# Performance work log

Measured on AMD Instinct MI355X. Metric: run time of the kernel, lower is better.

The kernel has to match this reference:

```python
import jax, jax.numpy as jnp
import numpy as np

N, B, T, D, H = 200, 100, 256, 5, 20  # count_lstms, batch, seq_len, io units, lstm units


def setup_inputs() -> dict:
    key = jax.random.key(0)
    ks = jax.random.split(key, 4)
    inputs = jax.random.normal(ks[0], (B, T, D), dtype=jnp.float32)
    # Stacked per-LSTM parameters (Keras gate order: i, f, c, o)
    W = jax.random.normal(ks[1], (N, D, 4 * H), dtype=jnp.float32) * (1.0 / np.sqrt(D))
    U = jax.random.normal(ks[2], (N, H, 4 * H), dtype=jnp.float32) * (1.0 / np.sqrt(H))
    b = jnp.zeros((N, 4 * H), dtype=jnp.float32)
    dense_W = jax.random.normal(ks[3], (N * H, D), dtype=jnp.float32) * (1.0 / np.sqrt(N * H))
    dense_b = jnp.zeros((D,), dtype=jnp.float32)
    return {"inputs": inputs, "W": W, "U": U, "b": b, "dense_W": dense_W, "dense_b": dense_b}


def reference(inputs, W, U, b, dense_W, dense_b):
    # inputs: [B, T, D]; W: [N, D, 4H]; U: [N, H, 4H]; b: [N, 4H]
    n, h = W.shape[0], U.shape[1]
    batch = inputs.shape[0]
    x_t = jnp.transpose(inputs, (1, 0, 2))  # [T, B, D]
    h0 = jnp.zeros((n, batch, h), dtype=inputs.dtype)
    c0 = jnp.zeros((n, batch, h), dtype=inputs.dtype)

    def step(carry, xt):
        hprev, cprev = carry
        # gates for all N lstms at once: [N, B, 4H]
        z = (jnp.einsum('bd,ndk->nbk', xt, W)
             + jnp.einsum('nbh,nhk->nbk', hprev, U)
             + b[:, None, :])
        zi, zf, zg, zo = jnp.split(z, 4, axis=-1)
        i = jax.nn.sigmoid(zi)
        f = jax.nn.sigmoid(zf)
        g = jnp.tanh(zg)
        o = jax.nn.sigmoid(zo)
        cnew = f * cprev + i * g
        hnew = o * jnp.tanh(cnew)
        return (hnew, cnew), hnew

    (_, _), hs = jax.lax.scan(step, (h0, c0), x_t)  # hs: [T, N, B, H]
    # concat along feature axis -> [B, T, N*H]
    concat = jnp.transpose(hs, (2, 0, 1, 3)).reshape(batch, x_t.shape[0], n * h)
    out = concat @ dense_W + dense_b  # [B, T, D]
    return out
```

## Files before the change

### kernel.cpp

```cpp
#include <hip/hip_runtime.h>
#include <math.h>

constexpr int NL = 200;
constexpr int B  = 100;
constexpr int T  = 256;
constexpr int D  = 5;
constexpr int H  = 20;
constexpr int NW = 7;
constexpr int KP = 40;
constexpr int NWAVE = 5;
constexpr int BLKT  = 64 * NWAVE;

constexpr int KX = 24;

typedef float  f32x4  __attribute__((ext_vector_type(4)));
typedef short  bf16x8 __attribute__((ext_vector_type(8)));

__device__ __forceinline__ float rcpf(float x) { return __builtin_amdgcn_rcpf(x); }

#if __has_builtin(__builtin_amdgcn_exp2f)
__device__ __forceinline__ float exp2fast(float x) { return __builtin_amdgcn_exp2f(x); }
#else
__device__ __forceinline__ float exp2fast(float x) { return __expf(x * 0.6931471805599453f); }
#endif

__device__ __forceinline__ unsigned short f2bf(float f) {
    union { float f; unsigned u; } v; v.f = f;
    unsigned r = v.u + 0x7fffu + ((v.u >> 16) & 1u);
    return (unsigned short)(r >> 16);
}

__device__ __forceinline__ void block_sync_lds() {
    asm volatile("s_waitcnt lgkmcnt(0)" ::: "memory");
    __builtin_amdgcn_s_barrier();
}

constexpr float NLOG2E = -1.4426950408889634f;
constexpr float TLOG2E = 2.8853900817779268f;

__global__ __launch_bounds__(256) void init_out_kernel(const float* __restrict__ dense_b,
                                                       float* __restrict__ out, int n) {
    int i = blockIdx.x * 256 + threadIdx.x;
    if (i < n) out[i] = dense_b[i % D];
}

template<bool USE_WS>
__global__ __attribute__((amdgpu_flat_work_group_size(BLKT, BLKT)))
void lstm_mfma5_kernel(
    const float* __restrict__ x,
    const float* __restrict__ Wg,
    const float* __restrict__ Ug,
    const float* __restrict__ bg,
    const float* __restrict__ dWg,
    float* __restrict__ pw,
    float* __restrict__ out)
{
    const int blk = blockIdx.x;
    const int n   = blk / NW;
    const int w   = blk % NW;
    const int tid = threadIdx.x;
    const int wid = tid >> 6;
    const int l   = tid & 63;
    const int c16 = l & 15;
    const int g4  = l >> 4;

    __shared__ __align__(16) short bcol[2][16][KP];

    for (int i = tid; i < 2 * 16 * KP / 2; i += BLKT)
        ((int*)&bcol[0][0][0])[i] = 0;

    const float* Un = Ug  + (size_t)n * H * 4 * H;
    const float* Wn = Wg  + (size_t)n * D * 4 * H;
    const float* bn = bg  + (size_t)n * 4 * H;
    const float* dn = dWg + (size_t)n * H * D;

    const int gateA = c16 & 3;
    const int hA4   = c16 >> 2;
    const float sA  = (gateA == 2) ? TLOG2E : NLOG2E;
    const int colA  = gateA * H + (wid * 4 + hA4);
    bf16x8 afrag;
    #pragma unroll
    for (int j = 0; j < 8; ++j) {
        const int k = 8 * g4 + j;
        float v = 0.0f;
        if (k < KX) {
            const int mt = k % 6, gg = k / 6;
            if (mt < 5) v = Un[(mt * 4 + gg) * 4 * H + colA];
        } else if (k < KX + D) {
            v = Wn[(k - KX) * 4 * H + colA];
        } else if (k == 30) {
            v = bn[colA];
        }
        afrag[j] = (short)f2bf(sA * v);
    }
    bf16x8 afrag_d = {};
    if (wid == 1) {
        #pragma unroll
        for (int j = 0; j < 8; ++j) {
            const int k = 8 * g4 + j;
            float v = 0.0f;
            if (c16 < D && k < KX) {
                const int mt = k % 6, gg = k / 6;
                if (mt < 5) v = dn[(mt * 4 + gg) * D + c16];
            }
            afrag_d[j] = (short)f2bf(v);
        }
    }

    const int  bgl    = w * 16 + c16;
    const bool bvalid = bgl < B;
    const float* xp   = x + (size_t)(bvalid ? bgl : 0) * T * D;
    float* pwn = USE_WS ? (pw + (size_t)n * T * (D * B))
                        : (out + ((size_t)bgl * T) * D);

    __syncthreads();

    float xn[D];
    if (wid == 0 && l < 16) {
        bf16x8 xb;
        #pragma unroll
        for (int d = 0; d < D; ++d) xb[d] = (short)f2bf(xp[d]);
        xb[5] = 0; xb[6] = (short)0x3F80; xb[7] = 0;
        *(bf16x8*)&bcol[0][c16][KX] = xb;
        const float* x1 = xp + (size_t)((T > 1) ? 1 : 0) * D;
        #pragma unroll
        for (int d = 0; d < D; ++d) xn[d] = x1[d];
    }
    __syncthreads();

    float cst = 0.0f;
    const f32x4 zero4 = {0.0f, 0.0f, 0.0f, 0.0f};
    int p = 0;

    for (int t = 0; t < T; ++t) {
        const bf16x8 bfrag = *(const bf16x8*)&bcol[p][c16][8 * g4];

        if (wid == 1) {
            const f32x4 accd = __builtin_amdgcn_mfma_f32_16x16x32_bf16(
                afrag_d, bfrag, zero4, 0, 0, 0);
            if (t > 0 && bvalid) {
                #pragma unroll
                for (int reg = 0; reg < 4; ++reg) {
                    const int d = g4 * 4 + reg;
                    if (d < D) {
                        if (USE_WS)
                            pwn[(size_t)(t - 1) * (D * B) + d * B + bgl] = accd[reg];
                        else
                            atomicAdd(&pwn[(size_t)(t - 1) * D + d], accd[reg]);
                    }
                }
            }
        }

        const f32x4 acc = __builtin_amdgcn_mfma_f32_16x16x32_bf16(
            afrag, bfrag, zero4, 0, 0, 0);
        const float iv = rcpf(1.0f + exp2fast(acc[0]));
        const float fv = rcpf(1.0f + exp2fast(acc[1]));
        const float gv = fmaf(-2.0f, rcpf(exp2fast(acc[2]) + 1.0f), 1.0f);
        const float ov = rcpf(1.0f + exp2fast(acc[3]));
        cst = fmaf(fv, cst, iv * gv);
        const float th = fmaf(-2.0f, rcpf(exp2fast(TLOG2E * cst) + 1.0f), 1.0f);
        const float hv = ov * th;

        bcol[p ^ 1][c16][g4 * 6 + wid] = (short)f2bf(hv);

        if (wid == 0 && l < 16) {
            bf16x8 xb;
            #pragma unroll
            for (int d = 0; d < D; ++d) xb[d] = (short)f2bf(xn[d]);
            xb[5] = 0; xb[6] = (short)0x3F80; xb[7] = 0;
            *(bf16x8*)&bcol[p ^ 1][c16][KX] = xb;
            const float* x2 = xp + (size_t)((t + 2 < T) ? t + 2 : T - 1) * D;
            #pragma unroll
            for (int d = 0; d < D; ++d) xn[d] = x2[d];
        }

        block_sync_lds();
        p ^= 1;
    }

    if (wid == 1) {
        const bf16x8 bfrag = *(const bf16x8*)&bcol[p][c16][8 * g4];
        const f32x4 accd = __builtin_amdgcn_mfma_f32_16x16x32_bf16(
            afrag_d, bfrag, zero4, 0, 0, 0);
        if (bvalid) {
            #pragma unroll
            for (int reg = 0; reg < 4; ++reg) {
                const int d = g4 * 4 + reg;
                if (d < D) {
                    if (USE_WS)
                        pwn[(size_t)(T - 1) * (D * B) + d * B + bgl] = accd[reg];
                    else
                        atomicAdd(&pwn[(size_t)(T - 1) * D + d], accd[reg]);
                }
            }
        }
    }
}

__global__ __launch_bounds__(512) void reduce_kernel(
    const float* __restrict__ pw, const float* __restrict__ dense_b,
    float* __restrict__ out)
{
    const int t    = blockIdx.x;
    const int flat = threadIdx.x;
    if (flat >= B * D) return;
    const int d = flat / B;
    const int b = flat % B;
    const float* p = pw + (size_t)t * (D * B) + flat;
    constexpr size_t stride = (size_t)T * D * B;
    float a0 = 0.0f, a1 = 0.0f;
    #pragma unroll 10
    for (int n = 0; n < NL; n += 2) {
        a0 += p[(size_t)n * stride];
        a1 += p[(size_t)(n + 1) * stride];
    }
    out[((size_t)b * T + t) * D + d] = a0 + a1 + dense_b[d];
}

extern "C" void kernel_launch(void* const* d_in, const int* in_sizes, int n_in,
                              void* d_out, int out_size, void* d_ws, size_t ws_size,
                              hipStream_t stream) {
    const float* x   = (const float*)d_in[0];
    const float* Wg  = (const float*)d_in[1];
    const float* Ug  = (const float*)d_in[2];
    const float* bg  = (const float*)d_in[3];
    const float* dWg = (const float*)d_in[4];
    const float* dbv = (const float*)d_in[5];
    float* out = (float*)d_out;

    const size_t need = (size_t)NL * T * D * B * sizeof(float);
    if (ws_size >= need) {
        float* pw = (float*)d_ws;
        lstm_mfma5_kernel<true><<<NL * NW, BLKT, 0, stream>>>(x, Wg, Ug, bg, dWg, pw, out);
        reduce_kernel<<<T, 512, 0, stream>>>(pw, dbv, out);
    } else {
        init_out_kernel<<<(out_size + 255) / 256, 256, 0, stream>>>(dbv, out, out_size);
        lstm_mfma5_kernel<false><<<NL * NW, BLKT, 0, stream>>>(x, Wg, Ug, bg, dWg, nullptr, out);
    }
}
```

Baseline: 230.0 us.

## Prepack inputs to bf16, read x from registers, spread dense projection

Adds a pre-kernel that packs each x row into a bf16 int4 with the bias-one slot included. The LSTM kernel now loads that packed row straight into the g4==3 lanes' MFMA B fragment, so x is no longer staged through LDS, and the LDS row shrinks to 24 halves. The dense output MFMA now runs in every wave, with each wave storing one output dimension instead of wave 1 storing all of them. It also uses a packed bf16 convert instruction and unrolls the time loop by two. The cost is an extra kernel launch, more workspace, and redundant MFMAs in the other waves.

```diff
diff --git a/kernel.cpp b/kernel.cpp
--- a/kernel.cpp
+++ b/kernel.cpp
@@ -7,11 +7,11 @@
 constexpr int D  = 5;
 constexpr int H  = 20;
 constexpr int NW = 7;
-constexpr int KP = 40;
+constexpr int KPH = 24;
 constexpr int NWAVE = 5;
 constexpr int BLKT  = 64 * NWAVE;
-
-constexpr int KX = 24;
+constexpr int BUFB  = 16 * KPH * 2;
+
 
 typedef float  f32x4  __attribute__((ext_vector_type(4)));
 typedef short  bf16x8 __attribute__((ext_vector_type(8)));
@@ -29,6 +29,9 @@
     unsigned r = v.u + 0x7fffu + ((v.u >> 16) & 1u);
     return (unsigned short)(r >> 16);
 }
+__device__ __forceinline__ unsigned pk2bf(float lo, float hi) {
+    return (unsigned)f2bf(lo) | ((unsigned)f2bf(hi) << 16);
+}
 
 __device__ __forceinline__ void block_sync_lds() {
     asm volatile("s_waitcnt lgkmcnt(0)" ::: "memory");
@@ -44,10 +47,23 @@
     if (i < n) out[i] = dense_b[i % D];
 }
 
+__global__ __launch_bounds__(256) void xpack_kernel(const float* __restrict__ x,
+                                                    int4* __restrict__ xp) {
+    int i = blockIdx.x * 256 + threadIdx.x;
+    if (i >= B * T) return;
+    const float* s = x + (size_t)i * D;
+    int4 v;
+    v.x = pk2bf(s[0], s[1]);
+    v.y = pk2bf(s[2], s[3]);
+    v.z = pk2bf(s[4], 0.0f);
+    v.w = 0x00003F80;
+    xp[i] = v;
+}
+
 template<bool USE_WS>
 __global__ __attribute__((amdgpu_flat_work_group_size(BLKT, BLKT)))
-void lstm_mfma5_kernel(
-    const float* __restrict__ x,
+void lstm5u_kernel(
+    const int4*  __restrict__ xp,
     const float* __restrict__ Wg,
     const float* __restrict__ Ug,
     const float* __restrict__ bg,
@@ -64,9 +80,9 @@
     const int c16 = l & 15;
     const int g4  = l >> 4;
 
-    __shared__ __align__(16) short bcol[2][16][KP];
-
-    for (int i = tid; i < 2 * 16 * KP / 2; i += BLKT)
+    __shared__ __align__(16) short bcol[2][16][KPH];
+
+    for (int i = tid; i < 2 * 16 * KPH / 2; i += BLKT)
         ((int*)&bcol[0][0][0])[i] = 0;
 
     const float* Un = Ug  + (size_t)n * H * 4 * H;
@@ -83,77 +99,66 @@
     for (int j = 0; j < 8; ++j) {
         const int k = 8 * g4 + j;
         float v = 0.0f;
-        if (k < KX) {
+        if (k < 24) {
             const int mt = k % 6, gg = k / 6;
             if (mt < 5) v = Un[(mt * 4 + gg) * 4 * H + colA];
-        } else if (k < KX + D) {
-            v = Wn[(k - KX) * 4 * H + colA];
+        } else if (k < 24 + D) {
+            v = Wn[(k - 24) * 4 * H + colA];
         } else if (k == 30) {
             v = bn[colA];
         }
         afrag[j] = (short)f2bf(sA * v);
     }
-    bf16x8 afrag_d = {};
-    if (wid == 1) {
-        #pragma unroll
-        for (int j = 0; j < 8; ++j) {
-            const int k = 8 * g4 + j;
-            float v = 0.0f;
-            if (c16 < D && k < KX) {
-                const int mt = k % 6, gg = k / 6;
-                if (mt < 5) v = dn[(mt * 4 + gg) * D + c16];
-            }
-            afrag_d[j] = (short)f2bf(v);
-        }
+    bf16x8 afd;
+    #pragma unroll
+    for (int j = 0; j < 8; ++j) {
+        const int k = 8 * g4 + j;
+        float v = 0.0f;
+        if (c16 < D && k < 24) {
+            const int mt = k % 6, gg = k / 6;
+            if (mt < 5) v = dn[(mt * 4 + gg) * D + c16];
+        }
+        afd[j] = (short)f2bf(v);
     }
 
     const int  bgl    = w * 16 + c16;
     const bool bvalid = bgl < B;
-    const float* xp   = x + (size_t)(bvalid ? bgl : 0) * T * D;
-    float* pwn = USE_WS ? (pw + (size_t)n * T * (D * B))
-                        : (out + ((size_t)bgl * T) * D);
+    const int4* xq = xp + (size_t)(bvalid ? bgl : 0) * T;
+
+    const bool dlane = bvalid && (g4 == (wid >> 2));
+    const int  dreg  = wid & 3;
+    float* pd = USE_WS ? (pw + (size_t)n * T * (D * B) + wid * B + bgl)
+                       : (out + ((size_t)bgl * T) * D + wid);
+
+    char* lb = (char*)&bcol[0][0][0];
+    const int rdoff = c16 * 48 + (g4 < 3 ? g4 * 16 : 32);
+    const int woff  = c16 * 48 + (g4 * 6 + wid) * 2;
 
     __syncthreads();
 
-    float xn[D];
-    if (wid == 0 && l < 16) {
-        bf16x8 xb;
-        #pragma unroll
-        for (int d = 0; d < D; ++d) xb[d] = (short)f2bf(xp[d]);
-        xb[5] = 0; xb[6] = (short)0x3F80; xb[7] = 0;
-        *(bf16x8*)&bcol[0][c16][KX] = xb;
-        const float* x1 = xp + (size_t)((T > 1) ? 1 : 0) * D;
-        #pragma unroll
-        for (int d = 0; d < D; ++d) xn[d] = x1[d];
-    }
-    __syncthreads();
-
+    int4 xf = xq[0];
     float cst = 0.0f;
-    const f32x4 zero4 = {0.0f, 0.0f, 0.0f, 0.0f};
-    int p = 0;
-
-    for (int t = 0; t < T; ++t) {
-        const bf16x8 bfrag = *(const bf16x8*)&bcol[p][c16][8 * g4];
-
-        if (wid == 1) {
-            const f32x4 accd = __builtin_amdgcn_mfma_f32_16x16x32_bf16(
-                afrag_d, bfrag, zero4, 0, 0, 0);
-            if (t > 0 && bvalid) {
-                #pragma unroll
-                for (int reg = 0; reg < 4; ++reg) {
-                    const int d = g4 * 4 + reg;
-                    if (d < D) {
-                        if (USE_WS)
-                            pwn[(size_t)(t - 1) * (D * B) + d * B + bgl] = accd[reg];
-                        else
-                            atomicAdd(&pwn[(size_t)(t - 1) * D + d], accd[reg]);
-                    }
-                }
-            }
-        }
-
-        const f32x4 acc = __builtin_amdgcn_mfma_f32_16x16x32_bf16(
-            afrag, bfrag, zero4, 0, 0, 0);
+    const f32x4 z4 = {0.0f, 0.0f, 0.0f, 0.0f};
+
+    auto step = [&](const int p, const int t) {
+        const int4 hvi = *(const int4*)(lb + p * BUFB + rdoff);
+        int4 bi;
+        bi.x = (g4 == 3) ? xf.x : hvi.x;
+        bi.y = (g4 == 3) ? xf.y : hvi.y;
+        bi.z = (g4 == 3) ? xf.z : hvi.z;
+        bi.w = (g4 == 3) ? xf.w : hvi.w;
+        union { int4 i; bf16x8 h; } u; u.i = bi;
+        const bf16x8 bfrag = u.h;
+
+        xf = xq[(t + 1 < T) ? t + 1 : T - 1];
+
+        const f32x4 accd = __builtin_amdgcn_mfma_f32_16x16x32_bf16(afd, bfrag, z4, 0, 0, 0);
+        if (t > 0 && dlane) {
+            if (USE_WS) pd[(size_t)(t - 1) * (D * B)] = accd[dreg];
+            else        atomicAdd(&pd[(size_t)(t - 1) * D], accd[dreg]);
+        }
+
+        const f32x4 acc = __builtin_amdgcn_mfma_f32_16x16x32_bf16(afrag, bfrag, z4, 0, 0, 0);
         const float iv = rcpf(1.0f + exp2fast(acc[0]));
         const float fv = rcpf(1.0f + exp2fast(acc[1]));
         const float gv = fmaf(-2.0f, rcpf(exp2fast(acc[2]) + 1.0f), 1.0f);
@@ -162,38 +167,22 @@
         const float th = fmaf(-2.0f, rcpf(exp2fast(TLOG2E * cst) + 1.0f), 1.0f);
         const float hv = ov * th;
 
-        bcol[p ^ 1][c16][g4 * 6 + wid] = (short)f2bf(hv);
-
-        if (wid == 0 && l < 16) {
-            bf16x8 xb;
-            #pragma unroll
-            for (int d = 0; d < D; ++d) xb[d] = (short)f2bf(xn[d]);
-            xb[5] = 0; xb[6] = (short)0x3F80; xb[7] = 0;
-            *(bf16x8*)&bcol[p ^ 1][c16][KX] = xb;
-            const float* x2 = xp + (size_t)((t + 2 < T) ? t + 2 : T - 1) * D;
-            #pragma unroll
-            for (int d = 0; d < D; ++d) xn[d] = x2[d];
-        }
+        unsigned hp;
+        asm("v_cvt_pk_bf16_f32 %0, %1, %2" : "=v"(hp) : "v"(hv), "v"(hv));
+        *(short*)(lb + (p ^ 1) * BUFB + woff) = (short)hp;
 
         block_sync_lds();
-        p ^= 1;
-    }
-
-    if (wid == 1) {
-        const bf16x8 bfrag = *(const bf16x8*)&bcol[p][c16][8 * g4];
-        const f32x4 accd = __builtin_amdgcn_mfma_f32_16x16x32_bf16(
-            afrag_d, bfrag, zero4, 0, 0, 0);
-        if (bvalid) {
-            #pragma unroll
-            for (int reg = 0; reg < 4; ++reg) {
-                const int d = g4 * 4 + reg;
-                if (d < D) {
-                    if (USE_WS)
-                        pwn[(size_t)(T - 1) * (D * B) + d * B + bgl] = accd[reg];
-                    else
-                        atomicAdd(&pwn[(size_t)(T - 1) * D + d], accd[reg]);
-                }
-            }
+    };
+
+    for (int t = 0; t < T; t += 2) { step(0, t); step(1, t + 1); }
+
+    {
+        const int4 hvi = *(const int4*)(lb + rdoff);
+        union { int4 i; bf16x8 h; } u; u.i = hvi;
+        const f32x4 accd = __builtin_amdgcn_mfma_f32_16x16x32_bf16(afd, u.h, z4, 0, 0, 0);
+        if (dlane) {
+            if (USE_WS) pd[(size_t)(T - 1) * (D * B)] = accd[dreg];
+            else        atomicAdd(&pd[(size_t)(T - 1) * D], accd[dreg]);
         }
     }
 }
@@ -229,13 +218,18 @@
     const float* dbv = (const float*)d_in[5];
     float* out = (float*)d_out;
 
-    const size_t need = (size_t)NL * T * D * B * sizeof(float);
-    if (ws_size >= need) {
-        float* pw = (float*)d_ws;
-        lstm_mfma5_kernel<true><<<NL * NW, BLKT, 0, stream>>>(x, Wg, Ug, bg, dWg, pw, out);
+    const size_t xpk_bytes = (size_t)B * T * sizeof(int4);
+    const size_t pw_bytes  = (size_t)NL * T * D * B * sizeof(float);
+
+    int4* xpk = (int4*)d_ws;
+    xpack_kernel<<<(B * T + 255) / 256, 256, 0, stream>>>(x, xpk);
+
+    if (ws_size >= xpk_bytes + pw_bytes) {
+        float* pw = (float*)((char*)d_ws + xpk_bytes);
+        lstm5u_kernel<true><<<NL * NW, BLKT, 0, stream>>>(xpk, Wg, Ug, bg, dWg, pw, out);
         reduce_kernel<<<T, 512, 0, stream>>>(pw, dbv, out);
     } else {
         init_out_kernel<<<(out_size + 255) / 256, 256, 0, stream>>>(dbv, out, out_size);
-        lstm_mfma5_kernel<false><<<NL * NW, BLKT, 0, stream>>>(x, Wg, Ug, bg, dWg, nullptr, out);
-    }
-}
+        lstm5u_kernel<false><<<NL * NW, BLKT, 0, stream>>>(xpk, Wg, Ug, bg, dWg, nullptr, out);
+    }
+}
```

Result: slower. 303.1 us (+31.8%).
